# Performance work log

Measured on AMD Instinct MI355X. Metric: run time of the kernel, lower is better.

## Reference

```python
import jax, jax.numpy as jnp
import numpy as np


def _mha(q, k, v, num_heads):
    # q,k,v: [B, L, C] -> multi-head attention, scale = 1/sqrt(head_dim)
    B, Lq, C = q.shape
    Lk = k.shape[1]
    d = C // num_heads
    qh = q.reshape(B, Lq, num_heads, d)
    kh = k.reshape(B, Lk, num_heads, d)
    vh = v.reshape(B, Lk, num_heads, d)
    scale = 1.0 / jnp.sqrt(jnp.asarray(d, q.dtype))
    scores = jnp.einsum('blhd,bmhd->bhlm', qh, kh) * scale
    probs = jax.nn.softmax(scores, axis=-1)
    out = jnp.einsum('bhlm,bmhd->blhd', probs, vh)
    return out.reshape(B, Lq, C)


def setup_inputs() -> dict:
    key = jax.random.key(0)
    ks = jax.random.split(key, 9)
    b, n, f, l, C = 1, 4, 8, 256, 320
    s = 0.02
    return {
        'hidden_states': jax.random.normal(ks[0], (b * n * f, l, C), jnp.float32),
        'Wq': jax.random.normal(ks[1], (C, C), jnp.float32) * s,
        'Wk': jax.random.normal(ks[2], (C, C), jnp.float32) * s,
        'Wv': jax.random.normal(ks[3], (C, C), jnp.float32) * s,
        'Wo': jax.random.normal(ks[4], (C, C), jnp.float32) * s,
        'bo': jnp.zeros((C,), jnp.float32),
        'Wq_i2v': jax.random.normal(ks[5], (C, C), jnp.float32) * s,
        'Wo_i2v': jax.random.normal(ks[6], (C, C), jnp.float32) * s,
        'bo_i2v': jnp.zeros((C,), jnp.float32),
        'num_heads': 8,
        'num_views': 4,
        'num_frames': 8,
    }


def reference(hidden_states, Wq, Wk, Wv, Wo, bo, Wq_i2v, Wo_i2v, bo_i2v,
              num_heads, num_views, num_frames):
    BNF, l, C = hidden_states.shape
    n, f = num_views, num_frames
    b = BNF // (n * f)
    # '(b n f) l c -> (b f) (n l) c'
    h = hidden_states.reshape(b, n, f, l, C).transpose(0, 2, 1, 3, 4).reshape(b * f, n * l, C)
    L = n * l

    q = h @ Wq
    k = h @ Wk
    v = h @ Wv

    # first-frame KV broadcast across all frames within the same b
    k_first = jnp.broadcast_to(k.reshape(b, f, L, C)[:, 0:1], (b, f, L, C)).reshape(b * f, L, C)
    v_first = jnp.broadcast_to(v.reshape(b, f, L, C)[:, 0:1], (b, f, L, C)).reshape(b * f, L, C)

    base = _mha(q, k, v, num_heads)

    q_i2v = h @ Wq_i2v
    i2v = _mha(q_i2v, k_first, v_first, num_heads)
    i2v = i2v @ Wo_i2v + bo_i2v

    out = (base + i2v) @ Wo + bo

    # '(b f) (n l) c -> (b n f) l c'
    out = out.reshape(b, f, n, l, C).transpose(0, 2, 1, 3, 4).reshape(b * n * f, l, C)
    return out
```

## Files before the change

kernel.cpp:

```cpp
#include <hip/hip_runtime.h>

#define MROWS 8192
#define CDIM  320
#define QPAD  512

typedef __attribute__((ext_vector_type(8))) short bf16x8;
typedef __attribute__((ext_vector_type(4))) float f32x4;

__device__ __forceinline__ unsigned bfbits(float x) {
  union { float f; unsigned u; } a; a.f = x;
  return a.u + 0x8000u;
}
__device__ __forceinline__ unsigned pack2bf(float a, float b) {
  return (bfbits(a) >> 16) | (bfbits(b) & 0xffff0000u);
}
__device__ __forceinline__ void splitbf(float x, short& hi, short& lo) {
  unsigned hu = bfbits(x) & 0xffff0000u;
  union { unsigned u; float f; } h; h.u = hu;
  hi = (short)(hu >> 16);
  lo = (short)(bfbits(x - h.f) >> 16);
}

__device__ __forceinline__ int swizzle_row(int r) {
  int ff = r >> 10;
  int t  = r & 1023;
  int nn = t >> 8;
  int ll = t & 255;
  return nn * 2048 + ff * 256 + ll;
}

__global__ __launch_bounds__(256) void wc_kernel(
    const float* __restrict__ Woi, const float* __restrict__ Wo,
    float* __restrict__ Wc)
{
  const int r0 = blockIdx.x * 64, c0 = blockIdx.y * 64;
  __shared__ float As[64][36];
  __shared__ float Bs[32][68];
  const int tid = threadIdx.x, tx = tid & 15, ty = tid >> 4;
  float acc[4][4] = {};

  const int ra = tid >> 3, kq = (tid & 7) * 4;
  const int kb = tid >> 4, cq = (tid & 15) * 4;

  for (int k0 = 0; k0 < 320; k0 += 32) {
    float4 a1 = *(const float4*)(Woi + (size_t)(r0 + ra) * 320 + k0 + kq);
    float4 a2 = *(const float4*)(Woi + (size_t)(r0 + ra + 32) * 320 + k0 + kq);
    float4 b1 = *(const float4*)(Wo + (size_t)(k0 + kb) * 320 + c0 + cq);
    float4 b2 = *(const float4*)(Wo + (size_t)(k0 + kb + 16) * 320 + c0 + cq);
    __syncthreads();
    *(float4*)&As[ra][kq] = a1;
    *(float4*)&As[ra + 32][kq] = a2;
    *(float4*)&Bs[kb][cq] = b1;
    *(float4*)&Bs[kb + 16][cq] = b2;
    __syncthreads();
    #pragma unroll
    for (int kk = 0; kk < 32; ++kk) {
      float4 bv = *(const float4*)&Bs[kk][tx * 4];
      #pragma unroll
      for (int i = 0; i < 4; ++i) {
        float a = As[ty * 4 + i][kk];
        acc[i][0] = fmaf(a, bv.x, acc[i][0]);
        acc[i][1] = fmaf(a, bv.y, acc[i][1]);
        acc[i][2] = fmaf(a, bv.z, acc[i][2]);
        acc[i][3] = fmaf(a, bv.w, acc[i][3]);
      }
    }
  }
  #pragma unroll
  for (int i = 0; i < 4; ++i) {
    float4 v = make_float4(acc[i][0], acc[i][1], acc[i][2], acc[i][3]);
    *(float4*)(Wc + (size_t)(r0 + ty * 4 + i) * 320 + c0 + tx * 4) = v;
  }
}

__global__ __launch_bounds__(256) void pack_kernel(
    const float* __restrict__ hidden,
    const float* __restrict__ Wq, const float* __restrict__ Wk,
    const float* __restrict__ Wv, const float* __restrict__ Wqi,
    const float* __restrict__ Wo, const float* __restrict__ Wc,
    const float* __restrict__ bo, const float* __restrict__ boi,
    short* __restrict__ Ah, short* __restrict__ Al,
    short* __restrict__ WTh, short* __restrict__ WTl,
    short* __restrict__ WFh, short* __restrict__ WFl,
    float* __restrict__ bc,
    short* __restrict__ Qp, short* __restrict__ Kp, short* __restrict__ Qip,
    float qscale)
{
  const int b = blockIdx.x, tid = threadIdx.x;
  if (b < 64) {
    const int r0 = b * 128;
    for (int e = tid; e < 128 * 80; e += 256) {
      int r = e / 80, cq = (e % 80) * 4;
      float4 x = *(const float4*)(hidden + (size_t)swizzle_row(r0 + r) * 320 + cq);
      union { ushort4 v; short s[4]; } h, l;
      splitbf(x.x, h.s[0], l.s[0]); splitbf(x.y, h.s[1], l.s[1]);
      splitbf(x.z, h.s[2], l.s[2]); splitbf(x.w, h.s[3], l.s[3]);
      *(ushort4*)&Ah[(size_t)(r0 + r) * 320 + cq] = h.v;
      *(ushort4*)&Al[(size_t)(r0 + r) * 320 + cq] = l.v;
    }
  } else if (b < 128) {
    const int t2 = b - 64, wi = t2 >> 4, seg = t2 & 15;
    const float* W = wi == 0 ? Wq : wi == 1 ? Wk : wi == 2 ? Wv : Wqi;
    const float s = (wi == 0 || wi == 3) ? qscale : 1.0f;
    short* th = WTh + (size_t)wi * 320 * 320;
    short* tl = WTl + (size_t)wi * 320 * 320;
    for (int e = tid; e < 20 * 320; e += 256) {
      int n = seg * 20 + e / 320, k = e % 320;
      short hi, lo;
      splitbf(W[(size_t)k * 320 + n] * s, hi, lo);
      th[(size_t)n * 320 + k] = hi;
      tl[(size_t)n * 320 + k] = lo;
    }
  } else if (b < 160) {
    const int t2 = b - 128;
    for (int e = tid; e < 10 * 640; e += 256) {
      int n = t2 * 10 + e / 640, k = e % 640;
      float x = (k < 320) ? Wo[(size_t)k * 320 + n] : Wc[(size_t)(k - 320) * 320 + n];
      short hi, lo;
      splitbf(x, hi, lo);
      WFh[(size_t)n * 640 + k] = hi;
      WFl[(size_t)n * 640 + k] = lo;
    }
  } else if (b < 168) {
    const int n = (b - 160) * 40 + tid;
    if (tid < 40) {
      float s = bo[n];
      for (int j = 0; j < 320; ++j) s = fmaf(boi[j], Wo[(size_t)j * 320 + n], s);
      bc[n] = s;
    }
  } else {
    const int bz = b - 168, buf = bz >> 5, seg = bz & 31;
    short* P = buf == 0 ? Qp : buf == 1 ? Kp : Qip;
    const uint4 z = make_uint4(0, 0, 0, 0);
    for (int e = tid; e < 256 * 24; e += 256) {
      int row = (seg << 8) + (e / 24);
      int cc = e % 24, h = cc / 3, c3 = cc % 3;
      *(uint4*)&P[(size_t)row * QPAD + h * 64 + 40 + c3 * 8] = z;
    }
  }
}

__global__ __launch_bounds__(256, 3) void mfma_gemm(
    const short* __restrict__ Ah, const short* __restrict__ Al,
    const short* __restrict__ BTh, const short* __restrict__ BTl,
    int K, int mode,
    short* __restrict__ Qp, short* __restrict__ Kp,
    short* __restrict__ Vt, short* __restrict__ Qip,
    float* __restrict__ Of, const float* __restrict__ bias)
{
  const int tid  = threadIdx.x;
  const int wave = tid >> 6;
  const int lane = tid & 63;
  const int quad = lane >> 4;
  const int l16  = lane & 15;
  const int row0 = blockIdx.x * 128;

  const short *bth, *btl;
  int nbase, wi = 0;
  if (mode == 0) {
    const int ct = blockIdx.y;
    wi = ct / 5;
    bth = BTh + (size_t)wi * 320 * 320;
    btl = BTl + (size_t)wi * 320 * 320;
    nbase = (ct % 5) * 64;
  } else {
    bth = BTh; btl = BTl;
    nbase = blockIdx.y * 64;
  }

  __shared__ short Ash[128][40], Asl[128][40];
  __shared__ short Bsh[64][40],  Bsl[64][40];

  f32x4 acc[2][4];
  #pragma unroll
  for (int mt = 0; mt < 2; ++mt)
    #pragma unroll
    for (int nt = 0; nt < 4; ++nt) acc[mt][nt] = (f32x4){0.f, 0.f, 0.f, 0.f};

  const int ar = tid >> 2, akc = (tid & 3) * 8;
  const int bn = tid >> 2, bkc = (tid & 3) * 8;

  const short* pa_h = Ah + (size_t)(row0 + ar) * K + akc;
  const short* pa_l = Al ? Al + (size_t)(row0 + ar) * K + akc : nullptr;
  const short* pb_h = bth + (size_t)(nbase + bn) * K + bkc;
  const short* pb_l = btl + (size_t)(nbase + bn) * K + bkc;

  for (int k0 = 0; k0 < K; k0 += 32) {
    uint4 ah1 = *(const uint4*)(pa_h + k0);
    uint4 ah2 = *(const uint4*)(pa_h + (size_t)64 * K + k0);
    uint4 al1, al2;
    if (Al) {
      al1 = *(const uint4*)(pa_l + k0);
      al2 = *(const uint4*)(pa_l + (size_t)64 * K + k0);
    }
    uint4 bh = *(const uint4*)(pb_h + k0);
    uint4 bl = *(const uint4*)(pb_l + k0);
    __syncthreads();
    *(uint4*)&Ash[ar][akc]      = ah1;
    *(uint4*)&Ash[ar + 64][akc] = ah2;
    if (Al) {
      *(uint4*)&Asl[ar][akc]      = al1;
      *(uint4*)&Asl[ar + 64][akc] = al2;
    }
    *(uint4*)&Bsh[bn][bkc] = bh;
    *(uint4*)&Bsl[bn][bkc] = bl;
    __syncthreads();

    bf16x8 afh[2], afl[2], bfh[4], bfl[4];
    #pragma unroll
    for (int mt = 0; mt < 2; ++mt) {
      afh[mt] = *(const bf16x8*)&Ash[wave * 32 + mt * 16 + l16][quad * 8];
      if (Al) afl[mt] = *(const bf16x8*)&Asl[wave * 32 + mt * 16 + l16][quad * 8];
    }
    #pragma unroll
    for (int nt = 0; nt < 4; ++nt) {
      bfh[nt] = *(const bf16x8*)&Bsh[nt * 16 + l16][quad * 8];
      bfl[nt] = *(const bf16x8*)&Bsl[nt * 16 + l16][quad * 8];
    }
    #pragma unroll
    for (int mt = 0; mt < 2; ++mt)
      #pragma unroll
      for (int nt = 0; nt < 4; ++nt) {
        acc[mt][nt] = __builtin_amdgcn_mfma_f32_16x16x32_bf16(afh[mt], bfh[nt], acc[mt][nt], 0, 0, 0);
        acc[mt][nt] = __builtin_amdgcn_mfma_f32_16x16x32_bf16(afh[mt], bfl[nt], acc[mt][nt], 0, 0, 0);
        if (Al)
          acc[mt][nt] = __builtin_amdgcn_mfma_f32_16x16x32_bf16(afl[mt], bfh[nt], acc[mt][nt], 0, 0, 0);
      }
  }

  if (mode == 0) {
    if (wi == 2) {
      #pragma unroll
      for (int mt = 0; mt < 2; ++mt)
        #pragma unroll
        for (int nt = 0; nt < 4; ++nt) {
          const int col  = nbase + nt * 16 + l16;
          const int rowb = row0 + wave * 32 + mt * 16 + quad * 4;
          union { ushort4 v; short s[4]; } pk;
          #pragma unroll
          for (int r = 0; r < 4; ++r) pk.s[r] = (short)(bfbits(acc[mt][nt][r]) >> 16);
          *(ushort4*)&Vt[(size_t)col * MROWS + rowb] = pk.v;
        }
    } else {
      short* Op = wi == 0 ? Qp : wi == 1 ? Kp : Qip;
      #pragma unroll
      for (int mt = 0; mt < 2; ++mt)
        #pragma unroll
        for (int nt = 0; nt < 4; ++nt) {
          const int col  = nbase + nt * 16 + l16;
          const int h    = col / 40;
          const int pcol = h * 64 + (col - h * 40);
          const int rowb = row0 + wave * 32 + mt * 16 + quad * 4;
          #pragma unroll
          for (int r = 0; r < 4; ++r)
            Op[(size_t)(rowb + r) * QPAD + pcol] = (short)(bfbits(acc[mt][nt][r]) >> 16);
        }
    }
  } else {
    #pragma unroll
    for (int mt = 0; mt < 2; ++mt)
      #pragma unroll
      for (int nt = 0; nt < 4; ++nt) {
        const int col  = nbase + nt * 16 + l16;
        const int rowb = row0 + wave * 32 + mt * 16 + quad * 4;
        const float bb = bias[col];
        #pragma unroll
        for (int r = 0; r < 4; ++r)
          Of[(size_t)swizzle_row(rowb + r) * CDIM + col] = acc[mt][nt][r] + bb;
      }
  }
}

__global__ __launch_bounds__(256, 4) void attn_kernel(
    const short* __restrict__ Qp, const short* __restrict__ Qip,
    const short* __restrict__ Kp, const short* __restrict__ Vtg,
    short* __restrict__ AOh)
{
  const int qblk = blockIdx.x;
  const int hh   = blockIdx.y;
  const int zz   = blockIdx.z;
  const int var  = zz >> 3;
  const int bf   = zz & 7;
  const int tid  = threadIdx.x;
  const int wave = tid >> 6;
  const int lane = tid & 63;
  const int quad = lane >> 4;
  const int l16  = lane & 15;

  const short* Q = var ? Qip : Qp;
  const int kvbase = var ? 0 : (bf << 10);
  const int coff = var * 320 + hh * 40;

  __shared__ short Ks[64][72];
  __shared__ short Vt[48][72];
  __shared__ short Ps[4][2][16][72];

  *(uint4*)&Ks[tid >> 2][40 + (tid & 3) * 8] = make_uint4(0, 0, 0, 0);
  if (tid < 64)
    *(uint4*)&Vt[40 + (tid >> 3)][(tid & 7) * 8] = make_uint4(0, 0, 0, 0);

  bf16x8 qf0[2], qf1[2];
  #pragma unroll
  for (int qt = 0; qt < 2; ++qt) {
    const short* qp = Q + (size_t)((bf << 10) + (qblk << 7) + (wave << 5) + (qt << 4) + l16) * QPAD + hh * 64;
    qf0[qt] = *(const bf16x8*)(qp + quad * 8);
    qf1[qt] = *(const bf16x8*)(qp + 32 + quad * 8);
  }

  f32x4 acc[2][3];
  float lsum[2] = {0.f, 0.f};
  #pragma unroll
  for (int qt = 0; qt < 2; ++qt)
    #pragma unroll
    for (int t = 0; t < 3; ++t) acc[qt][t] = (f32x4){0.f, 0.f, 0.f, 0.f};

  const short* Kb = Kp + (size_t)kvbase * QPAD + hh * 64;
  const short* Vb = Vtg + (size_t)(hh * 40) * MROWS + kvbase;

  const int k1 = tid / 5, c1 = tid % 5;
  const short* g1 = Kb + (size_t)k1 * QPAD + c1 * 8;
  short*       s1 = &Ks[k1][c1 * 8];
  const short* g2; short* s2; int inc2;
  if (tid < 64) {
    int u = tid + 256, k2 = u / 5, c2 = u % 5;
    g2 = Kb + (size_t)k2 * QPAD + c2 * 8;
    s2 = &Ks[k2][c2 * 8];
    inc2 = 64 * QPAD;
  } else {
    int v = tid - 64;
    g2 = Vb + (size_t)(v >> 3) * MROWS + (v & 7) * 8;
    s2 = &Vt[v >> 3][(v & 7) * 8];
    inc2 = 64;
  }
  const short* g3 = nullptr; short* s3 = nullptr;
  if (tid < 128) {
    int v = tid + 192;
    g3 = Vb + (size_t)(v >> 3) * MROWS + (v & 7) * 8;
    s3 = &Vt[v >> 3][(v & 7) * 8];
  }

  uint4 r1 = *(const uint4*)g1;
  uint4 r2 = *(const uint4*)g2;
  uint4 r3 = make_uint4(0, 0, 0, 0);
  if (tid < 128) r3 = *(const uint4*)g3;

  for (int step = 0; step < 16; ++step) {
    __syncthreads();
    *(uint4*)s1 = r1;
    *(uint4*)s2 = r2;
    if (tid < 128) *(uint4*)s3 = r3;
    __syncthreads();

    g1 += (size_t)64 * QPAD;
    g2 += inc2;
    r1 = *(const uint4*)g1;
    r2 = *(const uint4*)g2;
    if (tid < 128) { g3 += 64; r3 = *(const uint4*)g3; }

    bf16x8 vf[2][3];
    #pragma unroll
    for (int kh = 0; kh < 2; ++kh)
      #pragma unroll
      for (int t = 0; t < 3; ++t)
        vf[kh][t] = *(const bf16x8*)&Vt[t * 16 + l16][kh * 32 + quad * 8];

    #pragma unroll
    for (int kt = 0; kt < 4; ++kt) {
      const short* kr = &Ks[kt * 16 + l16][quad * 8];
      bf16x8 kb0 = *(const bf16x8*)kr;
      bf16x8 kb1 = *(const bf16x8*)(kr + 32);
      #pragma unroll
      for (int qt = 0; qt < 2; ++qt) {
        f32x4 st = (f32x4){0.f, 0.f, 0.f, 0.f};
        st = __builtin_amdgcn_mfma_f32_16x16x32_bf16(kb0, qf0[qt], st, 0, 0, 0);
        st = __builtin_amdgcn_mfma_f32_16x16x32_bf16(kb1, qf1[qt], st, 0, 0, 0);
        float p0 = __expf(st[0]);
        float p1 = __expf(st[1]);
        float p2 = __expf(st[2]);
        float p3 = __expf(st[3]);
        lsum[qt] += (p0 + p1) + (p2 + p3);
        uint2 pk;
        pk.x = pack2bf(p0, p1);
        pk.y = pack2bf(p2, p3);
        *(uint2*)&Ps[wave][qt][l16][kt * 16 + quad * 4] = pk;
      }
    }

    asm volatile("s_waitcnt lgkmcnt(0)" ::: "memory");

    #pragma unroll
    for (int qt = 0; qt < 2; ++qt) {
      bf16x8 pa0 = *(const bf16x8*)&Ps[wave][qt][l16][quad * 8];
      bf16x8 pa1 = *(const bf16x8*)&Ps[wave][qt][l16][32 + quad * 8];
      #pragma unroll
      for (int t = 0; t < 3; ++t) {
        acc[qt][t] = __builtin_amdgcn_mfma_f32_16x16x32_bf16(pa0, vf[0][t], acc[qt][t], 0, 0, 0);
        acc[qt][t] = __builtin_amdgcn_mfma_f32_16x16x32_bf16(pa1, vf[1][t], acc[qt][t], 0, 0, 0);
      }
    }
  }

  #pragma unroll
  for (int qt = 0; qt < 2; ++qt) {
    float li = lsum[qt];
    li += __shfl_xor(li, 16);
    li += __shfl_xor(li, 32);
    float inv = 1.f / li;
    float invr[4];
    #pragma unroll
    for (int r = 0; r < 4; ++r) invr[r] = __shfl(inv, quad * 4 + r, 64);

    const int baserow = (bf << 10) + (qblk << 7) + (wave << 5) + (qt << 4) + quad * 4;
    #pragma unroll
    for (int t = 0; t < 3; ++t) {
      int dcol = t * 16 + l16;
      if (dcol < 40) {
        short* op = AOh + (size_t)baserow * 640 + coff + dcol;
        #pragma unroll
        for (int r = 0; r < 4; ++r)
          op[(size_t)r * 640] = (short)(bfbits(acc[qt][t][r] * invr[r]) >> 16);
      }
    }
  }
}

extern "C" void kernel_launch(void* const* d_in, const int* in_sizes, int n_in,
                              void* d_out, int out_size, void* d_ws, size_t ws_size,
                              hipStream_t stream) {
  const float* hidden  = (const float*)d_in[0];
  const float* Wq      = (const float*)d_in[1];
  const float* Wk      = (const float*)d_in[2];
  const float* Wv      = (const float*)d_in[3];
  const float* Wo      = (const float*)d_in[4];
  const float* bo      = (const float*)d_in[5];
  const float* Wq_i2v  = (const float*)d_in[6];
  const float* Wo_i2v  = (const float*)d_in[7];
  const float* bo_i2v  = (const float*)d_in[8];
  float* out = (float*)d_out;

  const size_t SZ  = (size_t)MROWS * CDIM;
  const size_t SZP = (size_t)MROWS * QPAD;
  short* Ah  = (short*)d_ws;
  short* Al  = Ah + SZ;
  short* AOh = Ah;
  short* Qp  = Al + SZ;
  short* Kp  = Qp + SZP;
  short* Qip = Kp + SZP;
  short* Vt  = Qip + SZP;
  short* WTh = Vt + (size_t)328 * MROWS;
  short* WTl = WTh + 409600;
  short* WFh = WTl + 409600;
  short* WFl = WFh + 204800;
  float* Wc  = (float*)(WFl + 204800);
  float* bc  = Wc + 102400;

  const float qscale = 0.15811388300841898f;

  wc_kernel<<<dim3(5, 5), 256, 0, stream>>>(Wo_i2v, Wo, Wc);

  pack_kernel<<<dim3(264), 256, 0, stream>>>(
      hidden, Wq, Wk, Wv, Wq_i2v, Wo, Wc, bo, bo_i2v,
      Ah, Al, WTh, WTl, WFh, WFl, bc, Qp, Kp, Qip, qscale);

  mfma_gemm<<<dim3(64, 20), 256, 0, stream>>>(
      Ah, Al, WTh, WTl, 320, 0, Qp, Kp, Vt, Qip, nullptr, nullptr);

  attn_kernel<<<dim3(8, 8, 16), 256, 0, stream>>>(Qp, Qip, Kp, Vt, AOh);

  mfma_gemm<<<dim3(64, 5), 256, 0, stream>>>(
      AOh, nullptr, WFh, WFl, 640, 1, nullptr, nullptr, nullptr, nullptr, out, bc);
}
```

Measured before the change: 227.2 us.

## Shrink per-wave P staging buffer and drop register prefetch of K/V tiles

Reorders the score loop so each query tile is finished before the next, which lets one 16x68 P buffer per wave replace the double-buffered one and cuts LDS and register use. It also removes the register prefetch of the next K/V tile, loading global data straight into shared memory just before the barrier. The aim is lower resource use and higher occupancy. The cost is that global-load latency is no longer hidden behind compute, and the 68-element row pitch breaks 16-byte alignment for the 128-bit LDS reads of P.

```diff
diff --git a/kernel.cpp b/kernel.cpp
--- a/kernel.cpp
+++ b/kernel.cpp
@@ -293,7 +293,7 @@
 
   __shared__ short Ks[64][72];
   __shared__ short Vt[48][72];
-  __shared__ short Ps[4][2][16][72];
+  __shared__ short Ps[4][16][68];
 
   *(uint4*)&Ks[tid >> 2][40 + (tid & 3) * 8] = make_uint4(0, 0, 0, 0);
   if (tid < 64)
@@ -320,12 +320,12 @@
   const int k1 = tid / 5, c1 = tid % 5;
   const short* g1 = Kb + (size_t)k1 * QPAD + c1 * 8;
   short*       s1 = &Ks[k1][c1 * 8];
-  const short* g2; short* s2; int inc2;
+  const short* g2; short* s2; size_t inc2;
   if (tid < 64) {
     int u = tid + 256, k2 = u / 5, c2 = u % 5;
     g2 = Kb + (size_t)k2 * QPAD + c2 * 8;
     s2 = &Ks[k2][c2 * 8];
-    inc2 = 64 * QPAD;
+    inc2 = (size_t)64 * QPAD;
   } else {
     int v = tid - 64;
     g2 = Vb + (size_t)(v >> 3) * MROWS + (v & 7) * 8;
@@ -339,23 +339,12 @@
     s3 = &Vt[v >> 3][(v & 7) * 8];
   }
 
-  uint4 r1 = *(const uint4*)g1;
-  uint4 r2 = *(const uint4*)g2;
-  uint4 r3 = make_uint4(0, 0, 0, 0);
-  if (tid < 128) r3 = *(const uint4*)g3;
-
   for (int step = 0; step < 16; ++step) {
     __syncthreads();
-    *(uint4*)s1 = r1;
-    *(uint4*)s2 = r2;
-    if (tid < 128) *(uint4*)s3 = r3;
-    __syncthreads();
-
-    g1 += (size_t)64 * QPAD;
-    g2 += inc2;
-    r1 = *(const uint4*)g1;
-    r2 = *(const uint4*)g2;
-    if (tid < 128) { g3 += 64; r3 = *(const uint4*)g3; }
+    *(uint4*)s1 = *(const uint4*)g1;  g1 += (size_t)64 * QPAD;
+    *(uint4*)s2 = *(const uint4*)g2;  g2 += inc2;
+    if (tid < 128) { *(uint4*)s3 = *(const uint4*)g3;  g3 += 64; }
+    __syncthreads();
 
     bf16x8 vf[2][3];
     #pragma unroll
@@ -365,12 +354,12 @@
         vf[kh][t] = *(const bf16x8*)&Vt[t * 16 + l16][kh * 32 + quad * 8];
 
     #pragma unroll
-    for (int kt = 0; kt < 4; ++kt) {
-      const short* kr = &Ks[kt * 16 + l16][quad * 8];
-      bf16x8 kb0 = *(const bf16x8*)kr;
-      bf16x8 kb1 = *(const bf16x8*)(kr + 32);
-      #pragma unroll
-      for (int qt = 0; qt < 2; ++qt) {
+    for (int qt = 0; qt < 2; ++qt) {
+      #pragma unroll
+      for (int kt = 0; kt < 4; ++kt) {
+        const short* kr = &Ks[kt * 16 + l16][quad * 8];
+        bf16x8 kb0 = *(const bf16x8*)kr;
+        bf16x8 kb1 = *(const bf16x8*)(kr + 32);
         f32x4 st = (f32x4){0.f, 0.f, 0.f, 0.f};
         st = __builtin_amdgcn_mfma_f32_16x16x32_bf16(kb0, qf0[qt], st, 0, 0, 0);
         st = __builtin_amdgcn_mfma_f32_16x16x32_bf16(kb1, qf1[qt], st, 0, 0, 0);
@@ -382,16 +371,13 @@
         uint2 pk;
         pk.x = pack2bf(p0, p1);
         pk.y = pack2bf(p2, p3);
-        *(uint2*)&Ps[wave][qt][l16][kt * 16 + quad * 4] = pk;
-      }
-    }
-
-    asm volatile("s_waitcnt lgkmcnt(0)" ::: "memory");
-
-    #pragma unroll
-    for (int qt = 0; qt < 2; ++qt) {
-      bf16x8 pa0 = *(const bf16x8*)&Ps[wave][qt][l16][quad * 8];
-      bf16x8 pa1 = *(const bf16x8*)&Ps[wave][qt][l16][32 + quad * 8];
+        *(uint2*)&Ps[wave][l16][kt * 16 + quad * 4] = pk;
+      }
+
+      asm volatile("s_waitcnt lgkmcnt(0)" ::: "memory");
+
+      bf16x8 pa0 = *(const bf16x8*)&Ps[wave][l16][quad * 8];
+      bf16x8 pa1 = *(const bf16x8*)&Ps[wave][l16][32 + quad * 8];
       #pragma unroll
       for (int t = 0; t < 3; ++t) {
         acc[qt][t] = __builtin_amdgcn_mfma_f32_16x16x32_bf16(pa0, vf[0][t], acc[qt][t], 0, 0, 0);
```

After: 213.7 us. 6.0% less time.
